# Kernel optimization log

Hardware: AMD Instinct MI355X
Metric: run time of the kernel (lower is better)

The kernel has to match this reference:

```python
import jax, jax.numpy as jnp
import numpy as np

EPS = 1e-5

def _round_ste(x):
    # straight-through round (identical value in fwd; STE grad in bwd module)
    return x + jax.lax.stop_gradient(jnp.round(x) - x)

def _quant_weight(w, bits):
    # per-tensor symmetric absmax quantization to `bits` bits (BitNet-style)
    qb = float(2 ** (bits - 1) - 1)
    scale = qb / jnp.maximum(jnp.max(jnp.abs(w)), EPS)
    return _round_ste(jnp.clip(w * scale, -qb, qb)) / scale

def _quant_act(x):
    # per-token 8-bit absmax activation quantization
    qb = 127.0
    scale = qb / jnp.maximum(jnp.max(jnp.abs(x), axis=-1, keepdims=True), EPS)
    return _round_ste(jnp.clip(x * scale, -qb, qb)) / scale

def _layernorm(x, gamma, beta):
    mu = jnp.mean(x, axis=-1, keepdims=True)
    var = jnp.mean(jnp.square(x - mu), axis=-1, keepdims=True)
    return (x - mu) * jax.lax.rsqrt(var + EPS) * gamma + beta

def _qlinear(x, w, b, bits):
    return jnp.einsum('btd,fd->btf', _quant_act(x), _quant_weight(w, bits)) + b

def setup_inputs() -> dict:
    key = jax.random.key(0)
    ks = jax.random.split(key, 4)
    B, T, D, F = 8, 2048, 1024, 4096
    return {
        'x': jax.random.normal(ks[0], (B, T, D), dtype=jnp.float32),
        'mask': jnp.ones((B, T, 1), dtype=jnp.float32),
        'ln_gamma': jnp.ones((D,), dtype=jnp.float32),
        'ln_beta': jnp.zeros((D,), dtype=jnp.float32),
        'w1': jax.random.normal(ks[1], (F, D), dtype=jnp.float32) * (1.0 / np.sqrt(D)),
        'b1': jnp.zeros((F,), dtype=jnp.float32),
        'w2': jax.random.normal(ks[2], (D, F), dtype=jnp.float32) * (1.0 / np.sqrt(F)),
        'b2': jnp.zeros((D,), dtype=jnp.float32),
        'bitwidth': 8,
    }

def reference(x, mask, ln_gamma, ln_beta, w1, b1, w2, b2, bitwidth):
    y = _layernorm(x, ln_gamma, ln_beta)           # [B,T,D]
    y = _qlinear(y, w1, b1, bitwidth)              # [B,T,F]
    y = y * jax.nn.sigmoid(y)                      # swish
    y = _qlinear(y, w2, b2, bitwidth)              # [B,T,D]
    seq_mask = mask[:, :, 0][..., None]            # [B,T,1]
    y = y * seq_mask
    return x + 0.5 * y
```

## Files before the change

kernel.cpp:

```cpp
#include <hip/hip_runtime.h>
#include <hip/hip_bf16.h>
#include <stdint.h>


typedef int v4i __attribute__((ext_vector_type(4)));
typedef int v16i __attribute__((ext_vector_type(16)));

#define BK 128

__device__ __forceinline__ float wave_max64(float v) {
#pragma unroll
  for (int off = 32; off; off >>= 1) v = fmaxf(v, __shfl_xor(v, off, 64));
  return v;
}

__device__ __forceinline__ void load16_to_lds(const int8_t* g, int8_t* l) {
  __builtin_amdgcn_global_load_lds((const __attribute__((address_space(1))) void*)g,
                                   (__attribute__((address_space(3))) void*)l, 16, 0, 0);
}

__global__ __launch_bounds__(256) void absmax_kernel(const float* __restrict__ w, int n4,
                                                     int* __restrict__ slot) {
  float m = 0.f;
  const float4* w4 = (const float4*)w;
  for (int i = blockIdx.x * 256 + threadIdx.x; i < n4; i += gridDim.x * 256) {
    float4 v = w4[i];
    m = fmaxf(fmaxf(fabsf(v.x), fabsf(v.y)), fmaxf(fmaxf(fabsf(v.z), fabsf(v.w)), m));
  }
  m = wave_max64(m);
  __shared__ float sm[4];
  int lane = threadIdx.x & 63, wv = threadIdx.x >> 6;
  if (!lane) sm[wv] = m;
  __syncthreads();
  if (!threadIdx.x) {
    m = fmaxf(fmaxf(sm[0], sm[1]), fmaxf(sm[2], sm[3]));
    atomicMax(slot, __float_as_int(m));
  }
}

__global__ void scales_kernel(const int* __restrict__ wmax, const int* __restrict__ bits,
                              float* __restrict__ scal) {
  float qb = (float)((1 << (bits[0] - 1)) - 1);
  scal[2] = qb / fmaxf(__int_as_float(wmax[0]), 1e-5f);
  scal[3] = qb / fmaxf(__int_as_float(wmax[1]), 1e-5f);
  scal[4] = qb;
}

__global__ __launch_bounds__(256) void wquant_kernel(const float* __restrict__ w,
                                                     const float* __restrict__ scal, int which,
                                                     int8_t* __restrict__ out) {
  float s = scal[2 + which], qb = scal[4];
  int i = blockIdx.x * 256 + threadIdx.x;
  float4 v = ((const float4*)w)[i];
  char4 q;
  q.x = (char)(int)rintf(fminf(fmaxf(v.x * s, -qb), qb));
  q.y = (char)(int)rintf(fminf(fmaxf(v.y * s, -qb), qb));
  q.z = (char)(int)rintf(fminf(fmaxf(v.z * s, -qb), qb));
  q.w = (char)(int)rintf(fminf(fmaxf(v.w * s, -qb), qb));
  ((char4*)out)[i] = q;
}

__global__ __launch_bounds__(256) void ln_quant_kernel(const float* __restrict__ x,
                                                       const float* __restrict__ gamma,
                                                       const float* __restrict__ beta,
                                                       int8_t* __restrict__ xq,
                                                       float* __restrict__ xscale) {
  const int row = blockIdx.x;
  const int tid = threadIdx.x;
  const float4 v = ((const float4*)(x + (size_t)row * 1024))[tid];
  float s = v.x + v.y + v.z + v.w;
  float ss = fmaf(v.x, v.x, fmaf(v.y, v.y, fmaf(v.z, v.z, v.w * v.w)));
#pragma unroll
  for (int off = 32; off; off >>= 1) {
    s += __shfl_xor(s, off, 64);
    ss += __shfl_xor(ss, off, 64);
  }
  __shared__ float sm[8];
  const int lane = tid & 63, wv = tid >> 6;
  if (!lane) { sm[wv] = s; sm[4 + wv] = ss; }
  __syncthreads();
  s = sm[0] + sm[1] + sm[2] + sm[3];
  ss = sm[4] + sm[5] + sm[6] + sm[7];
  const float mu = s * (1.f / 1024.f);
  const float var = ss * (1.f / 1024.f) - mu * mu;
  const float rstd = rsqrtf(var + 1e-5f);
  const float4 g = ((const float4*)gamma)[tid];
  const float4 bb = ((const float4*)beta)[tid];
  float y0 = (v.x - mu) * rstd * g.x + bb.x;
  float y1 = (v.y - mu) * rstd * g.y + bb.y;
  float y2 = (v.z - mu) * rstd * g.z + bb.z;
  float y3 = (v.w - mu) * rstd * g.w + bb.w;
  float am = fmaxf(fmaxf(fabsf(y0), fabsf(y1)), fmaxf(fabsf(y2), fabsf(y3)));
  am = wave_max64(am);
  __syncthreads();
  if (!lane) sm[wv] = am;
  __syncthreads();
  am = fmaxf(fmaxf(sm[0], sm[1]), fmaxf(sm[2], sm[3]));
  const float scale = 127.f / fmaxf(am, 1e-5f);
  char4 q;
  q.x = (char)(int)rintf(fminf(fmaxf(y0 * scale, -127.f), 127.f));
  q.y = (char)(int)rintf(fminf(fmaxf(y1 * scale, -127.f), 127.f));
  q.z = (char)(int)rintf(fminf(fmaxf(y2 * scale, -127.f), 127.f));
  q.w = (char)(int)rintf(fminf(fmaxf(y3 * scale, -127.f), 127.f));
  ((char4*)(xq + (size_t)row * 1024))[tid] = q;
  if (!tid) xscale[row] = scale;
}

__global__ __launch_bounds__(256) void hquant_kernel(const ushort* __restrict__ h,
                                                     int8_t* __restrict__ hq,
                                                     float* __restrict__ hscale) {
  const int row = blockIdx.x;
  const int tid = threadIdx.x;
  const int4* p = (const int4*)(h + (size_t)row * 4096);
  union { int4 i4; ushort u[8]; } ua, ub;
  ua.i4 = p[tid * 2];
  ub.i4 = p[tid * 2 + 1];
  float f[16];
#pragma unroll
  for (int i = 0; i < 8; ++i) f[i] = __uint_as_float((unsigned)ua.u[i] << 16);
#pragma unroll
  for (int i = 0; i < 8; ++i) f[8 + i] = __uint_as_float((unsigned)ub.u[i] << 16);
  float am = 0.f;
#pragma unroll
  for (int i = 0; i < 16; ++i) am = fmaxf(am, fabsf(f[i]));
  am = wave_max64(am);
  __shared__ float sm[4];
  const int lane = tid & 63, wv = tid >> 6;
  if (!lane) sm[wv] = am;
  __syncthreads();
  am = fmaxf(fmaxf(sm[0], sm[1]), fmaxf(sm[2], sm[3]));
  const float scale = 127.f / fmaxf(am, 1e-5f);
  union { int4 i4; char c[16]; } q;
#pragma unroll
  for (int i = 0; i < 16; ++i)
    q.c[i] = (char)(int)rintf(fminf(fmaxf(f[i] * scale, -127.f), 127.f));
  ((int4*)(hq + (size_t)row * 4096))[tid] = q.i4;
  if (!tid) hscale[row] = scale;
}

template <int K, int BMt, int BNt>
__device__ __forceinline__ void gemm_core(const int8_t* __restrict__ A,
                                          const int8_t* __restrict__ B, int8_t* As, int8_t* Bs,
                                          v16i (&acc)[BMt / 64][BNt / 64]) {
  constexpr int AM = BMt / 64, AN = BNt / 64;
  const int tid = threadIdx.x;
  const int lane = tid & 63;
  const int wave = tid >> 6;
  const int wm = (wave & 1) * (BMt / 2);
  const int wn = (wave >> 1) * (BNt / 2);
  const int lrow = lane & 31;
  const int half = lane >> 5;
  const int x7 = lrow & 7;
  const size_t m0 = (size_t)blockIdx.y * BMt;
  const size_t n0 = (size_t)blockIdx.x * BNt;

  const int r = tid >> 3;
  const int cs = ((tid & 7) ^ (r & 7)) << 4;
  const int8_t* ga = A + (m0 + r) * K + cs;
  const int8_t* gb = B + (n0 + r) * K + cs;
  int8_t* la = As + tid * 16;
  int8_t* lb = Bs + tid * 16;

  for (int k0 = 0; k0 < K; k0 += BK) {
    __syncthreads();
#pragma unroll
    for (int t = 0; t < BMt / 32; ++t)
      load16_to_lds(ga + (size_t)(t * 32) * K + k0, la + t * 4096);
#pragma unroll
    for (int t = 0; t < BNt / 32; ++t)
      load16_to_lds(gb + (size_t)(t * 32) * K + k0, lb + t * 4096);
    __syncthreads();
#pragma unroll
    for (int ks = 0; ks < 4; ++ks) {
      const int so = ((ks * 2 + half) ^ x7) << 4;
      v4i af[AM], bf[AN];
#pragma unroll
      for (int i = 0; i < AM; ++i)
        af[i] = *(const v4i*)(As + (wm + i * 32 + lrow) * 128 + so);
#pragma unroll
      for (int j = 0; j < AN; ++j)
        bf[j] = *(const v4i*)(Bs + (wn + j * 32 + lrow) * 128 + so);
#pragma unroll
      for (int i = 0; i < AM; ++i)
#pragma unroll
        for (int j = 0; j < AN; ++j)
          acc[i][j] = __builtin_amdgcn_mfma_i32_32x32x32_i8(af[i], bf[j], acc[i][j], 0, 0, 0);
    }
  }
}

__global__ __launch_bounds__(256, 2) void gemm1_kernel(const int8_t* __restrict__ Aq,
                                                       const int8_t* __restrict__ Bq,
                                                       const float* __restrict__ xscale,
                                                       const float* __restrict__ scal,
                                                       const float* __restrict__ bias,
                                                       ushort* __restrict__ H) {
  __shared__ __align__(16) int8_t As[128 * 128];
  __shared__ __align__(16) int8_t Bs[256 * 128];
  v16i acc[2][4] = {};
  gemm_core<1024, 128, 256>(Aq, Bq, As, Bs, acc);
  const float sw1 = scal[2];
  const int lane = threadIdx.x & 63;
  const int wave = threadIdx.x >> 6;
  const int m0 = blockIdx.y * 128 + (wave & 1) * 64;
  const int n0 = blockIdx.x * 256 + (wave >> 1) * 128;
  const int cn = lane & 31;
  const int h4 = (lane >> 5) << 2;
#pragma unroll
  for (int i = 0; i < 2; ++i) {
#pragma unroll
    for (int reg = 0; reg < 16; ++reg) {
      const int row = (reg & 3) + ((reg >> 2) << 3) + h4;
      const int m = m0 + i * 32 + row;
      const float rcp = 1.0f / (xscale[m] * sw1);
#pragma unroll
      for (int j = 0; j < 4; ++j) {
        const int n = n0 + j * 32 + cn;
        const float v = (float)acc[i][j][reg] * rcp + bias[n];
        const float hsw = v / (1.0f + __expf(-v));
        __hip_bfloat16 hb = __float2bfloat16(hsw);
        H[(size_t)m * 4096 + n] = *(const ushort*)&hb;
      }
    }
  }
}

__global__ __launch_bounds__(256, 2) void gemm2_kernel(const int8_t* __restrict__ Aq,
                                                       const int8_t* __restrict__ Bq,
                                                       const float* __restrict__ hscale,
                                                       const float* __restrict__ scal,
                                                       const float* __restrict__ bias,
                                                       const float* __restrict__ x,
                                                       const float* __restrict__ mask,
                                                       float* __restrict__ out) {
  __shared__ __align__(16) int8_t As[256 * 128];
  __shared__ __align__(16) int8_t Bs[128 * 128];
  v16i acc[4][2] = {};
  gemm_core<4096, 256, 128>(Aq, Bq, As, Bs, acc);
  const float sw2 = scal[3];
  const int lane = threadIdx.x & 63;
  const int wave = threadIdx.x >> 6;
  const int m0 = blockIdx.y * 256 + (wave & 1) * 128;
  const int n0 = blockIdx.x * 128 + (wave >> 1) * 64;
  const int cn = lane & 31;
  const int h4 = (lane >> 5) << 2;
#pragma unroll
  for (int i = 0; i < 4; ++i) {
#pragma unroll
    for (int reg = 0; reg < 16; ++reg) {
      const int row = (reg & 3) + ((reg >> 2) << 3) + h4;
      const int m = m0 + i * 32 + row;
      const float rcp = 1.0f / (hscale[m] * sw2);
      const float mk = 0.5f * mask[m];
#pragma unroll
      for (int j = 0; j < 2; ++j) {
        const int n = n0 + j * 32 + cn;
        const float v = (float)acc[i][j][reg] * rcp + bias[n];
        const size_t idx = (size_t)m * 1024 + n;
        out[idx] = x[idx] + mk * v;
      }
    }
  }
}

extern "C" void kernel_launch(void* const* d_in, const int* in_sizes, int n_in, void* d_out,
                              int out_size, void* d_ws, size_t ws_size, hipStream_t stream) {
  const float* x = (const float*)d_in[0];
  const float* mask = (const float*)d_in[1];
  const float* gamma = (const float*)d_in[2];
  const float* beta = (const float*)d_in[3];
  const float* w1 = (const float*)d_in[4];
  const float* b1 = (const float*)d_in[5];
  const float* w2 = (const float*)d_in[6];
  const float* b2 = (const float*)d_in[7];
  const int* bits = (const int*)d_in[8];
  float* out = (float*)d_out;

  char* ws = (char*)d_ws;
  int* wmax = (int*)ws;
  float* scal = (float*)ws;
  float* xscale = (float*)(ws + (1u << 20));
  float* hscale = (float*)(ws + (2u << 20));
  int8_t* w1q = (int8_t*)(ws + (4u << 20));
  int8_t* w2q = (int8_t*)(ws + (8u << 20));
  int8_t* xq = (int8_t*)(ws + (12u << 20));
  int8_t* hq = (int8_t*)(ws + (28u << 20));
  ushort* h = (ushort*)(ws + (size_t)(92u << 20));

  const int NW = 4096 * 1024;

  absmax_kernel<<<1024, 256, 0, stream>>>(w1, NW / 4, wmax + 0);
  absmax_kernel<<<1024, 256, 0, stream>>>(w2, NW / 4, wmax + 1);
  scales_kernel<<<1, 1, 0, stream>>>(wmax, bits, scal);
  wquant_kernel<<<NW / 1024, 256, 0, stream>>>(w1, scal, 0, w1q);
  wquant_kernel<<<NW / 1024, 256, 0, stream>>>(w2, scal, 1, w2q);
  ln_quant_kernel<<<16384, 256, 0, stream>>>(x, gamma, beta, xq, xscale);
  gemm1_kernel<<<dim3(4096 / 256, 16384 / 128), 256, 0, stream>>>(xq, w1q, xscale, scal, b1, h);
  hquant_kernel<<<16384, 256, 0, stream>>>(h, hq, hscale);
  gemm2_kernel<<<dim3(1024 / 128, 16384 / 256), 256, 0, stream>>>(hq, w2q, hscale, scal, b2, x,
                                                                  mask, out);
}
```

Baseline: 439.0 us.

## Double-buffer GEMM LDS tiles with BK=64 and precompute dequant scales

The shared GEMM core now uses two LDS buffers with a K-tile of 64 instead of a single 128-wide tile. The next tile's global-to-LDS load is issued before the current tile's MFMAs, and one barrier per iteration replaces two. The swizzle changes to 4-way to match the narrower rows. Per-row and per-weight dequant factors are stored as reciprocals, so the epilogues use an FMA instead of a division, and swish uses a fast rcp. Risks: only one barrier guards buffer reuse while async LDS loads are in flight, and the smaller K step adds loop overhead.

Measured after the change: 501.3 us. 14.2% more time.

```diff
diff --git a/kernel.cpp b/kernel.cpp
--- a/kernel.cpp
+++ b/kernel.cpp
@@ -5,8 +5,6 @@
 
 typedef int v4i __attribute__((ext_vector_type(4)));
 typedef int v16i __attribute__((ext_vector_type(16)));
-
-#define BK 128
 
 __device__ __forceinline__ float wave_max64(float v) {
 #pragma unroll
@@ -41,9 +39,13 @@
 __global__ void scales_kernel(const int* __restrict__ wmax, const int* __restrict__ bits,
                               float* __restrict__ scal) {
   float qb = (float)((1 << (bits[0] - 1)) - 1);
-  scal[2] = qb / fmaxf(__int_as_float(wmax[0]), 1e-5f);
-  scal[3] = qb / fmaxf(__int_as_float(wmax[1]), 1e-5f);
+  float m1 = fmaxf(__int_as_float(wmax[0]), 1e-5f);
+  float m2 = fmaxf(__int_as_float(wmax[1]), 1e-5f);
+  scal[2] = qb / m1;
+  scal[3] = qb / m2;
   scal[4] = qb;
+  scal[5] = m1 / qb;
+  scal[6] = m2 / qb;
 }
 
 __global__ __launch_bounds__(256) void wquant_kernel(const float* __restrict__ w,
@@ -64,7 +66,7 @@
                                                        const float* __restrict__ gamma,
                                                        const float* __restrict__ beta,
                                                        int8_t* __restrict__ xq,
-                                                       float* __restrict__ xscale) {
+                                                       float* __restrict__ xdq) {
   const int row = blockIdx.x;
   const int tid = threadIdx.x;
   const float4 v = ((const float4*)(x + (size_t)row * 1024))[tid];
@@ -95,20 +97,20 @@
   __syncthreads();
   if (!lane) sm[wv] = am;
   __syncthreads();
-  am = fmaxf(fmaxf(sm[0], sm[1]), fmaxf(sm[2], sm[3]));
-  const float scale = 127.f / fmaxf(am, 1e-5f);
+  am = fmaxf(fmaxf(fmaxf(sm[0], sm[1]), fmaxf(sm[2], sm[3])), 1e-5f);
+  const float scale = 127.f / am;
   char4 q;
   q.x = (char)(int)rintf(fminf(fmaxf(y0 * scale, -127.f), 127.f));
   q.y = (char)(int)rintf(fminf(fmaxf(y1 * scale, -127.f), 127.f));
   q.z = (char)(int)rintf(fminf(fmaxf(y2 * scale, -127.f), 127.f));
   q.w = (char)(int)rintf(fminf(fmaxf(y3 * scale, -127.f), 127.f));
   ((char4*)(xq + (size_t)row * 1024))[tid] = q;
-  if (!tid) xscale[row] = scale;
+  if (!tid) xdq[row] = am * (1.f / 127.f);
 }
 
 __global__ __launch_bounds__(256) void hquant_kernel(const ushort* __restrict__ h,
                                                      int8_t* __restrict__ hq,
-                                                     float* __restrict__ hscale) {
+                                                     float* __restrict__ hdq) {
   const int row = blockIdx.x;
   const int tid = threadIdx.x;
   const int4* p = (const int4*)(h + (size_t)row * 4096);
@@ -128,14 +130,14 @@
   const int lane = tid & 63, wv = tid >> 6;
   if (!lane) sm[wv] = am;
   __syncthreads();
-  am = fmaxf(fmaxf(sm[0], sm[1]), fmaxf(sm[2], sm[3]));
-  const float scale = 127.f / fmaxf(am, 1e-5f);
+  am = fmaxf(fmaxf(fmaxf(sm[0], sm[1]), fmaxf(sm[2], sm[3])), 1e-5f);
+  const float scale = 127.f / am;
   union { int4 i4; char c[16]; } q;
 #pragma unroll
   for (int i = 0; i < 16; ++i)
     q.c[i] = (char)(int)rintf(fminf(fmaxf(f[i] * scale, -127.f), 127.f));
   ((int4*)(hq + (size_t)row * 4096))[tid] = q.i4;
-  if (!tid) hscale[row] = scale;
+  if (!tid) hdq[row] = am * (1.f / 127.f);
 }
 
 template <int K, int BMt, int BNt>
@@ -143,6 +145,7 @@
                                           const int8_t* __restrict__ B, int8_t* As, int8_t* Bs,
                                           v16i (&acc)[BMt / 64][BNt / 64]) {
   constexpr int AM = BMt / 64, AN = BNt / 64;
+  constexpr int NI = K / 64;
   const int tid = threadIdx.x;
   const int lane = tid & 63;
   const int wave = tid >> 6;
@@ -150,56 +153,62 @@
   const int wn = (wave >> 1) * (BNt / 2);
   const int lrow = lane & 31;
   const int half = lane >> 5;
-  const int x7 = lrow & 7;
+  const int x3 = lrow & 3;
   const size_t m0 = (size_t)blockIdx.y * BMt;
   const size_t n0 = (size_t)blockIdx.x * BNt;
 
-  const int r = tid >> 3;
-  const int cs = ((tid & 7) ^ (r & 7)) << 4;
+  const int r = tid >> 2;
+  const int cs = ((tid & 3) ^ (r & 3)) << 4;
   const int8_t* ga = A + (m0 + r) * K + cs;
   const int8_t* gb = B + (n0 + r) * K + cs;
-  int8_t* la = As + tid * 16;
-  int8_t* lb = Bs + tid * 16;
-
-  for (int k0 = 0; k0 < K; k0 += BK) {
+
+  auto stage = [&](int k0, int bi) {
+    int8_t* la = As + bi * (BMt * 64) + tid * 16;
+    int8_t* lb = Bs + bi * (BNt * 64) + tid * 16;
+#pragma unroll
+    for (int t = 0; t < BMt / 64; ++t)
+      load16_to_lds(ga + (size_t)(t * 64) * K + k0, la + t * 4096);
+#pragma unroll
+    for (int t = 0; t < BNt / 64; ++t)
+      load16_to_lds(gb + (size_t)(t * 64) * K + k0, lb + t * 4096);
+  };
+
+  stage(0, 0);
+  for (int i = 0; i < NI; ++i) {
     __syncthreads();
-#pragma unroll
-    for (int t = 0; t < BMt / 32; ++t)
-      load16_to_lds(ga + (size_t)(t * 32) * K + k0, la + t * 4096);
-#pragma unroll
-    for (int t = 0; t < BNt / 32; ++t)
-      load16_to_lds(gb + (size_t)(t * 32) * K + k0, lb + t * 4096);
-    __syncthreads();
-#pragma unroll
-    for (int ks = 0; ks < 4; ++ks) {
-      const int so = ((ks * 2 + half) ^ x7) << 4;
+    if (i + 1 < NI) stage((i + 1) * 64, (i + 1) & 1);
+    const int8_t* Ab = As + (i & 1) * (BMt * 64);
+    const int8_t* Bb = Bs + (i & 1) * (BNt * 64);
+#pragma unroll
+    for (int ks = 0; ks < 2; ++ks) {
+      const int so = ((ks * 2 + half) ^ x3) << 4;
       v4i af[AM], bf[AN];
 #pragma unroll
-      for (int i = 0; i < AM; ++i)
-        af[i] = *(const v4i*)(As + (wm + i * 32 + lrow) * 128 + so);
+      for (int ii = 0; ii < AM; ++ii)
+        af[ii] = *(const v4i*)(Ab + (wm + ii * 32 + lrow) * 64 + so);
 #pragma unroll
       for (int j = 0; j < AN; ++j)
-        bf[j] = *(const v4i*)(Bs + (wn + j * 32 + lrow) * 128 + so);
-#pragma unroll
-      for (int i = 0; i < AM; ++i)
+        bf[j] = *(const v4i*)(Bb + (wn + j * 32 + lrow) * 64 + so);
+#pragma unroll
+      for (int ii = 0; ii < AM; ++ii)
 #pragma unroll
         for (int j = 0; j < AN; ++j)
-          acc[i][j] = __builtin_amdgcn_mfma_i32_32x32x32_i8(af[i], bf[j], acc[i][j], 0, 0, 0);
+          acc[ii][j] = __builtin_amdgcn_mfma_i32_32x32x32_i8(af[ii], bf[j], acc[ii][j], 0, 0, 0);
     }
   }
 }
 
 __global__ __launch_bounds__(256, 2) void gemm1_kernel(const int8_t* __restrict__ Aq,
                                                        const int8_t* __restrict__ Bq,
-                                                       const float* __restrict__ xscale,
+                                                       const float* __restrict__ xdq,
                                                        const float* __restrict__ scal,
                                                        const float* __restrict__ bias,
                                                        ushort* __restrict__ H) {
-  __shared__ __align__(16) int8_t As[128 * 128];
-  __shared__ __align__(16) int8_t Bs[256 * 128];
+  __shared__ __align__(16) int8_t As[2 * 128 * 64];
+  __shared__ __align__(16) int8_t Bs[2 * 256 * 64];
   v16i acc[2][4] = {};
   gemm_core<1024, 128, 256>(Aq, Bq, As, Bs, acc);
-  const float sw1 = scal[2];
+  const float wdq = scal[5];
   const int lane = threadIdx.x & 63;
   const int wave = threadIdx.x >> 6;
   const int m0 = blockIdx.y * 128 + (wave & 1) * 64;
@@ -212,12 +221,12 @@
     for (int reg = 0; reg < 16; ++reg) {
       const int row = (reg & 3) + ((reg >> 2) << 3) + h4;
       const int m = m0 + i * 32 + row;
-      const float rcp = 1.0f / (xscale[m] * sw1);
+      const float dq = xdq[m] * wdq;
 #pragma unroll
       for (int j = 0; j < 4; ++j) {
         const int n = n0 + j * 32 + cn;
-        const float v = (float)acc[i][j][reg] * rcp + bias[n];
-        const float hsw = v / (1.0f + __expf(-v));
+        const float v = fmaf((float)acc[i][j][reg], dq, bias[n]);
+        const float hsw = v * __builtin_amdgcn_rcpf(1.0f + __expf(-v));
         __hip_bfloat16 hb = __float2bfloat16(hsw);
         H[(size_t)m * 4096 + n] = *(const ushort*)&hb;
       }
@@ -227,17 +236,17 @@
 
 __global__ __launch_bounds__(256, 2) void gemm2_kernel(const int8_t* __restrict__ Aq,
                                                        const int8_t* __restrict__ Bq,
-                                                       const float* __restrict__ hscale,
+                                                       const float* __restrict__ hdq,
                                                        const float* __restrict__ scal,
                                                        const float* __restrict__ bias,
                                                        const float* __restrict__ x,
                                                        const float* __restrict__ mask,
                                                        float* __restrict__ out) {
-  __shared__ __align__(16) int8_t As[256 * 128];
-  __shared__ __align__(16) int8_t Bs[128 * 128];
+  __shared__ __align__(16) int8_t As[2 * 256 * 64];
+  __shared__ __align__(16) int8_t Bs[2 * 128 * 64];
   v16i acc[4][2] = {};
   gemm_core<4096, 256, 128>(Aq, Bq, As, Bs, acc);
-  const float sw2 = scal[3];
+  const float wdq = scal[6];
   const int lane = threadIdx.x & 63;
   const int wave = threadIdx.x >> 6;
   const int m0 = blockIdx.y * 256 + (wave & 1) * 128;
@@ -250,14 +259,14 @@
     for (int reg = 0; reg < 16; ++reg) {
       const int row = (reg & 3) + ((reg >> 2) << 3) + h4;
       const int m = m0 + i * 32 + row;
-      const float rcp = 1.0f / (hscale[m] * sw2);
+      const float dq = hdq[m] * wdq;
       const float mk = 0.5f * mask[m];
 #pragma unroll
       for (int j = 0; j < 2; ++j) {
         const int n = n0 + j * 32 + cn;
-        const float v = (float)acc[i][j][reg] * rcp + bias[n];
+        const float v = fmaf((float)acc[i][j][reg], dq, bias[n]);
         const size_t idx = (size_t)m * 1024 + n;
-        out[idx] = x[idx] + mk * v;
+        out[idx] = fmaf(mk, v, x[idx]);
       }
     }
   }
@@ -279,8 +288,8 @@
   char* ws = (char*)d_ws;
   int* wmax = (int*)ws;
   float* scal = (float*)ws;
-  float* xscale = (float*)(ws + (1u << 20));
-  float* hscale = (float*)(ws + (2u << 20));
+  float* xdq = (float*)(ws + (1u << 20));
+  float* hdq = (float*)(ws + (2u << 20));
   int8_t* w1q = (int8_t*)(ws + (4u << 20));
   int8_t* w2q = (int8_t*)(ws + (8u << 20));
   int8_t* xq = (int8_t*)(ws + (12u << 20));
@@ -294,9 +303,9 @@
   scales_kernel<<<1, 1, 0, stream>>>(wmax, bits, scal);
   wquant_kernel<<<NW / 1024, 256, 0, stream>>>(w1, scal, 0, w1q);
   wquant_kernel<<<NW / 1024, 256, 0, stream>>>(w2, scal, 1, w2q);
-  ln_quant_kernel<<<16384, 256, 0, stream>>>(x, gamma, beta, xq, xscale);
-  gemm1_kernel<<<dim3(4096 / 256, 16384 / 128), 256, 0, stream>>>(xq, w1q, xscale, scal, b1, h);
-  hquant_kernel<<<16384, 256, 0, stream>>>(h, hq, hscale);
-  gemm2_kernel<<<dim3(1024 / 128, 16384 / 256), 256, 0, stream>>>(hq, w2q, hscale, scal, b2, x,
+  ln_quant_kernel<<<16384, 256, 0, stream>>>(x, gamma, beta, xq, xdq);
+  gemm1_kernel<<<dim3(4096 / 256, 16384 / 128), 256, 0, stream>>>(xq, w1q, xdq, scal, b1, h);
+  hquant_kernel<<<16384, 256, 0, stream>>>(h, hq, hdq);
+  gemm2_kernel<<<dim3(1024 / 128, 16384 / 256), 256, 0, stream>>>(hq, w2q, hdq, scal, b2, x,
                                                                   mask, out);
 }
```
